# Kernel optimization log

Hardware: AMD Instinct MI355X
Metric: run time of the kernel (lower is better)

The kernel has to match this reference:

```python
import jax, jax.numpy as jnp
import numpy as np
import math

B, S, H = 4, 4096, 64
WINDOW = 2


def setup_inputs() -> dict:
    key = jax.random.key(0)
    ks = jax.random.split(key, 7)
    s = 0.05
    return {
        "feature": jax.random.normal(ks[0], (B, S, H), dtype=jnp.float32),
        "Wq": jax.random.normal(ks[1], (H, H), dtype=jnp.float32) * s,
        "bq": jax.random.normal(ks[2], (H,), dtype=jnp.float32) * s,
        "Wk": jax.random.normal(ks[3], (H, H), dtype=jnp.float32) * s,
        "bk": jax.random.normal(ks[4], (H,), dtype=jnp.float32) * s,
        "Wv": jax.random.normal(ks[5], (H, H), dtype=jnp.float32) * s,
        "bv": jax.random.normal(ks[6], (H,), dtype=jnp.float32) * s,
    }


def reference(feature, Wq, bq, Wk, bk, Wv, bv):
    b, seq, d_k = feature.shape
    # torch nn.Linear: y = x @ W.T + b
    q = feature @ Wq.T + bq  # [B,S,H]
    k = feature @ Wk.T + bk
    v = feature @ Wv.T + bv

    # banded 0/1 mask, |i-j| <= window, then softmax over the FULL row
    # (faithful to the original: zeros outside the band also get exp(0)=1 weight)
    idx = jnp.arange(seq)
    band = (jnp.abs(idx[:, None] - idx[None, :]) <= WINDOW).astype(jnp.float32)  # [S,S]
    weights = jax.nn.softmax(band, axis=-1)  # [S,S]

    # locally-averaged K: weights @ k, shared across batch
    mixed_k = jnp.einsum('st,bth->bsh', weights, k)  # [B,S,H]
    scores = jnp.einsum('bsh,bth->bst', q, mixed_k) / math.sqrt(d_k)  # [B,S,S]
    attn = jax.nn.softmax(scores, axis=-1)
    out = jnp.einsum('bst,bth->bsh', attn, v)  # [B,S,H]
    return out
```

## Files before the change

### kernel.cpp

```cpp
#include <hip/hip_runtime.h>
#include <hip/hip_bf16.h>
#include <math.h>

#define SEQ 4096
#define HD  64
#define NBATCH 4

#define EM1   1.71828182845904523536f
#define INVD5 (1.0f/(4096.f + 5.f*EM1))
#define INVD4 (1.0f/(4096.f + 4.f*EM1))
#define INVD3 (1.0f/(4096.f + 3.f*EM1))

typedef __attribute__((ext_vector_type(8))) short short8;
typedef __attribute__((ext_vector_type(4))) short short4v;
typedef __attribute__((ext_vector_type(4))) float f32x4;

__device__ __forceinline__ f32x4 mfma16(short8 a, short8 b, f32x4 c) {
    return __builtin_amdgcn_mfma_f32_16x16x32_bf16(a, b, c, 0, 0, 0);
}

__device__ __forceinline__ short bfs(float x) {
    __hip_bfloat16 h = __float2bfloat16(x);
    return *(short*)&h;
}

__device__ __forceinline__ float sf(short s) {
    __hip_bfloat16 h;
    *(short*)&h = s;
    return __bfloat162float(h);
}

__device__ __forceinline__ short8 pack8(float4 a, float4 b) {
    short8 r;
    r[0] = bfs(a.x); r[1] = bfs(a.y); r[2] = bfs(a.z); r[3] = bfs(a.w);
    r[4] = bfs(b.x); r[5] = bfs(b.y); r[6] = bfs(b.z); r[7] = bfs(b.w);
    return r;
}

__device__ __forceinline__ float b2f(__hip_bfloat16 h) { return __bfloat162float(h); }

#define WSTR 72

__global__ __launch_bounds__(512, 4) void projm_kernel(
    const float* __restrict__ feat,
    const float* __restrict__ Wq, const float* __restrict__ Wk,
    const float* __restrict__ Wv,
    const float* __restrict__ bq, const float* __restrict__ bk,
    const float* __restrict__ bv,
    __hip_bfloat16* __restrict__ qsb, float* __restrict__ kpart,
    float* __restrict__ vpart, __hip_bfloat16* __restrict__ Mpart,
    float* __restrict__ kedge)
{
    __shared__ __hip_bfloat16 WbL[3 * 64 * WSTR];
    __shared__ __hip_bfloat16 kT[64 * 40];
    __shared__ __hip_bfloat16 vT[64 * 40];
    __shared__ __hip_bfloat16 lvt[64 * 40];
    __shared__ float kred[2][64];
    __shared__ float vred[2][64];

    const int tid  = threadIdx.x;
    const int wv   = tid >> 6, lane = tid & 63;
    const int rh   = wv & 1;
    const int role = wv >> 1;
    const int quad = lane >> 4, ln = lane & 15;
    const int R0 = blockIdx.x * 32;
    const int b  = R0 >> 12;
    const int t0 = R0 & (SEQ - 1);
    const int chunk = blockIdx.x & 127;

    short8 af0, af1;
    const bool hflag = (rh == 0) ? (t0 > 0) : (t0 < SEQ - 32);
    if (role < 3) {
        const float* fp = feat + (size_t)(R0 + rh * 16 + ln) * HD + quad * 8;
        af0 = pack8(*(const float4*)(fp),      *(const float4*)(fp + 4));
        af1 = pack8(*(const float4*)(fp + 32), *(const float4*)(fp + 36));
    } else {
        const int hrow = (rh == 0) ? (t0 - 2 + ln) : (t0 + 32 + ln);
        if (ln < 2 && hflag) {
            const float* fp = feat + ((size_t)(b << 12) + hrow) * HD + quad * 8;
            af0 = pack8(*(const float4*)(fp),      *(const float4*)(fp + 4));
            af1 = pack8(*(const float4*)(fp + 32), *(const float4*)(fp + 36));
        } else {
            #pragma unroll
            for (int j = 0; j < 8; ++j) { af0[j] = 0; af1[j] = 0; }
        }
    }

    {
        const int r = tid >> 3, c = (tid & 7) * 8;
        #pragma unroll
        for (int m = 0; m < 3; ++m) {
            const float* W = (m == 0) ? Wq : (m == 1) ? Wk : Wv;
            const float s = (m == 0) ? 0.125f : 1.f;
            const float* src = W + r * 64 + c;
            float4 a0 = *(const float4*)(src);
            float4 a1 = *(const float4*)(src + 4);
            a0.x*=s; a0.y*=s; a0.z*=s; a0.w*=s;
            a1.x*=s; a1.y*=s; a1.z*=s; a1.w*=s;
            *(short8*)(WbL + m * 64 * WSTR + r * WSTR + c) = pack8(a0, a1);
        }
    }
    __syncthreads();

    if (role == 0) {
        #pragma unroll
        for (int ct = 0; ct < 4; ++ct) {
            const int col = ct * 16 + ln;
            const __hip_bfloat16* wp = WbL + col * WSTR + quad * 8;
            short8 b0 = *(const short8*)(wp);
            short8 b1 = *(const short8*)(wp + 32);
            f32x4 c = {};
            c = mfma16(af0, b0, c);
            c = mfma16(af1, b1, c);
            const float bl = bq[col] * 0.125f;
            #pragma unroll
            for (int rr = 0; rr < 4; ++rr)
                qsb[(size_t)(R0 + rh * 16 + quad * 4 + rr) * HD + col] =
                    __float2bfloat16(c[rr] + bl);
        }
    } else if (role == 1) {
        #pragma unroll
        for (int ct = 0; ct < 4; ++ct) {
            const int col = ct * 16 + ln;
            const __hip_bfloat16* wp = WbL + 64 * WSTR + col * WSTR + quad * 8;
            short8 b0 = *(const short8*)(wp);
            short8 b1 = *(const short8*)(wp + 32);
            f32x4 c = {};
            c = mfma16(af0, b0, c);
            c = mfma16(af1, b1, c);
            float tot = c[0] + c[1] + c[2] + c[3];
            tot += __shfl_xor(tot, 16);
            tot += __shfl_xor(tot, 32);
            if (quad == 0) kred[rh][col] = tot;
            const float bl = bk[col];
            #pragma unroll
            for (int rr = 0; rr < 4; ++rr)
                kT[col * 40 + rh * 16 + quad * 4 + rr] =
                    __float2bfloat16(c[rr] + bl);
        }
    } else if (role == 2) {
        #pragma unroll
        for (int ct = 0; ct < 4; ++ct) {
            const int col = ct * 16 + ln;
            const __hip_bfloat16* wp = WbL + 2 * 64 * WSTR + col * WSTR + quad * 8;
            short8 b0 = *(const short8*)(wp);
            short8 b1 = *(const short8*)(wp + 32);
            f32x4 c = {};
            c = mfma16(af0, b0, c);
            c = mfma16(af1, b1, c);
            float tot = c[0] + c[1] + c[2] + c[3];
            tot += __shfl_xor(tot, 16);
            tot += __shfl_xor(tot, 32);
            if (quad == 0) vred[rh][col] = tot;
            const float bl = bv[col];
            #pragma unroll
            for (int rr = 0; rr < 4; ++rr)
                vT[col * 40 + 2 + rh * 16 + quad * 4 + rr] =
                    __float2bfloat16(c[rr] + bl);
        }
    } else {
        #pragma unroll
        for (int ct = 0; ct < 4; ++ct) {
            const int col = ct * 16 + ln;
            const __hip_bfloat16* wp = WbL + 2 * 64 * WSTR + col * WSTR + quad * 8;
            short8 b0 = *(const short8*)(wp);
            short8 b1 = *(const short8*)(wp + 32);
            f32x4 hc = {};
            hc = mfma16(af0, b0, hc);
            hc = mfma16(af1, b1, hc);
            if (quad == 0) {
                const float bl = bv[col];
                const int base = (rh == 0) ? 0 : 34;
                vT[col * 40 + base]     = __float2bfloat16(hflag ? hc[0] + bl : 0.f);
                vT[col * 40 + base + 1] = __float2bfloat16(hflag ? hc[1] + bl : 0.f);
            }
        }
    }
    __syncthreads();

    if (tid < 64) {
        kpart[(size_t)blockIdx.x * 64 + tid] =
            kred[0][tid] + kred[1][tid] + 32.f * bk[tid];
        vpart[(size_t)blockIdx.x * 64 + tid] =
            vred[0][tid] + vred[1][tid] + 32.f * bv[tid];
    }

    {
        const int h = tid & 63;
        const int tb = (tid >> 6) * 4;
        short4v u0 = *(const short4v*)&vT[h * 40 + tb];
        short4v u1 = *(const short4v*)&vT[h * 40 + tb + 4];
        float w[8];
        #pragma unroll
        for (int j = 0; j < 4; ++j) {
            w[j]     = sf(u0[j]);
            w[j + 4] = sf(u1[j]);
        }
        #pragma unroll
        for (int i = 0; i < 4; ++i)
            lvt[h * 40 + tb + i] =
                __float2bfloat16(w[i] + w[i+1] + w[i+2] + w[i+3] + w[i+4]);
    }

    if (chunk == 0) {
        if (tid < 256) {
            const int t = tid >> 6, h = tid & 63;
            kedge[b * 512 + t * 64 + h] = b2f(kT[h * 40 + t]);
        }
    } else if (chunk == 127) {
        if (tid < 256) {
            const int t = tid >> 6, h = tid & 63;
            kedge[b * 512 + (4 + t) * 64 + h] = b2f(kT[h * 40 + 28 + t]);
        }
    }
    __syncthreads();

    {
        __hip_bfloat16* mp = Mpart + (size_t)(b * 128 + chunk) * 4096;
        const int strip = wv >> 1;
        const int cth   = wv & 1;
        short8 a = *(const short8*)&kT[(strip * 16 + ln) * 40 + quad * 8];
        #pragma unroll
        for (int i = 0; i < 2; ++i) {
            const int ct = cth * 2 + i;
            short8 bb = *(const short8*)&lvt[(ct * 16 + ln) * 40 + quad * 8];
            f32x4 acc = {};
            acc = mfma16(a, bb, acc);
            #pragma unroll
            for (int rr = 0; rr < 4; ++rr)
                mp[(strip * 16 + quad * 4 + rr) * 64 + ct * 16 + ln] =
                    __float2bfloat16(acc[rr]);
        }
    }
}

__global__ __launch_bounds__(256) void redprep_kernel(
    const __hip_bfloat16* __restrict__ Mpart, const float* __restrict__ kpart,
    const float* __restrict__ vpart, const float* __restrict__ kedge,
    __hip_bfloat16* __restrict__ MTm, float* __restrict__ mktotF,
    float* __restrict__ ktotF, float* __restrict__ VDs,
    float* __restrict__ VtotF)
{
    const int b = blockIdx.y, x = blockIdx.x;
    const int tid = threadIdx.x;

    if (x < 32) {
        __shared__ float part[16][132];
        const int gl = tid >> 4;
        const int s  = tid & 15;
        const int e  = x * 128 + gl * 8;
        const __hip_bfloat16* src =
            Mpart + ((size_t)b * 128 + s * 8) * 4096 + e;
        float sum[8] = {0.f,0.f,0.f,0.f,0.f,0.f,0.f,0.f};
        #pragma unroll
        for (int c = 0; c < 8; ++c) {
            short8 v = *(const short8*)(src + (size_t)c * 4096);
            #pragma unroll
            for (int j = 0; j < 8; ++j) sum[j] += sf(v[j]);
        }
        #pragma unroll
        for (int j = 0; j < 8; ++j) part[s][gl * 8 + j] = sum[j];
        __syncthreads();
        if (tid < 128) {
            float t = 0.f;
            #pragma unroll
            for (int ss = 0; ss < 16; ++ss) t += part[ss][tid];
            const int e2 = x * 128 + tid;
            const int h1 = e2 >> 6, h2 = e2 & 63;
            MTm[(size_t)b * 4096 + h2 * 64 + h1] =
                __float2bfloat16((EM1 * INVD5) * t);
        }
        return;
    }

    __shared__ float red[4][64];
    __shared__ float red2[4][64];
    const int g = tid >> 6, h2 = tid & 63;
    {
        float kp = 0.f, vp = 0.f;
        for (int j = 0; j < 32; ++j) {
            kp += kpart[(size_t)(b * 128 + g * 32 + j) * 64 + h2];
            vp += vpart[(size_t)(b * 128 + g * 32 + j) * 64 + h2];
        }
        red[g][h2] = kp;
        red2[g][h2] = vp;
    }
    __syncthreads();
    if (tid < 64) {
        const int hh = tid;
        const float kt = red[0][hh] + red[1][hh] + red[2][hh] + red[3][hh];
        const float vt = red2[0][hh] + red2[1][hh] + red2[2][hh] + red2[3][hh];
        const float e0 = kedge[b * 512 + 0 * 64 + hh];
        const float e1 = kedge[b * 512 + 1 * 64 + hh];
        const float e2 = kedge[b * 512 + 2 * 64 + hh];
        const float e3 = kedge[b * 512 + 3 * 64 + hh];
        const float f0 = kedge[b * 512 + 4 * 64 + hh];
        const float f1 = kedge[b * 512 + 5 * 64 + hh];
        const float f2 = kedge[b * 512 + 6 * 64 + hh];
        const float f3 = kedge[b * 512 + 7 * 64 + hh];
        const float Sint = 5.f*kt - 4.f*e0 - 3.f*e1 - 2.f*e2 - e3
                         - f0 - 2.f*f1 - 3.f*f2 - 4.f*f3;
        const float SlocD = Sint * INVD5
                          + (e0+e1+e2 + f1+f2+f3) * INVD3
                          + (e0+e1+e2+e3 + f0+f1+f2+f3) * INVD4;
        mktotF[b * 64 + hh] = kt * (4092.f*INVD5 + 2.f*INVD4 + 2.f*INVD3) + EM1 * SlocD;
        ktotF[b * 64 + hh]  = kt;
        VDs[b * 64 + hh]    = INVD5 * vt;
        VtotF[b * 64 + hh]  = vt;
    }
}

__global__ __launch_bounds__(128) void out_kernel(
    const __hip_bfloat16* __restrict__ qsb, const __hip_bfloat16* __restrict__ MTm,
    const float* __restrict__ mktotF, const float* __restrict__ ktotF,
    const float* __restrict__ VDs, const float* __restrict__ VtotF,
    float* __restrict__ out)
{
    const int tid = threadIdx.x;
    const int wv = tid >> 6, lane = tid & 63;
    const int quad = lane >> 4, ln = lane & 15;
    const int R0 = blockIdx.x * 16;
    const int b = R0 >> 12;

    short8 qa0, qa1;
    {
        const __hip_bfloat16* qp = qsb + (size_t)(R0 + ln) * HD + quad * 8;
        qa0 = *(const short8*)qp;
        qa1 = *(const short8*)(qp + 32);
    }

    const __hip_bfloat16* mtb = MTm + (size_t)b * 4096;
    f32x4 acc[2];
    #pragma unroll
    for (int i = 0; i < 2; ++i) {
        const int ct = wv * 2 + i;
        short8 b0 = *(const short8*)(mtb + (ct * 16 + ln) * 64 + quad * 8);
        short8 b1 = *(const short8*)(mtb + (ct * 16 + ln) * 64 + 32 + quad * 8);
        f32x4 c = {};
        c = mfma16(qa0, b0, c);
        c = mfma16(qa1, b1, c);
        acc[i] = c;
    }

    short8 mk0, mk1, kt0, kt1;
    #pragma unroll
    for (int j = 0; j < 8; ++j) {
        mk0[j] = bfs(mktotF[b * 64 + quad * 8 + j]);
        mk1[j] = bfs(mktotF[b * 64 + 32 + quad * 8 + j]);
        kt0[j] = bfs(ktotF[b * 64 + quad * 8 + j]);
        kt1[j] = bfs(ktotF[b * 64 + 32 + quad * 8 + j]);
    }
    f32x4 accd = {}, acck = {};
    accd = mfma16(qa0, mk0, accd);
    accd = mfma16(qa1, mk1, accd);
    acck = mfma16(qa0, kt0, acck);
    acck = mfma16(qa1, kt1, acck);

    float vt[2], vd[2];
    #pragma unroll
    for (int i = 0; i < 2; ++i) {
        const int ct = wv * 2 + i;
        vt[i] = VtotF[b * 64 + ct * 16 + ln];
        vd[i] = VDs[b * 64 + ct * 16 + ln];
    }

    float inv[4];
    #pragma unroll
    for (int r = 0; r < 4; ++r) inv[r] = 1.f / (4096.f + accd[r]);

    #pragma unroll
    for (int i = 0; i < 2; ++i)
        #pragma unroll
        for (int r = 0; r < 4; ++r)
            out[(size_t)(R0 + quad * 4 + r) * HD + (wv * 2 + i) * 16 + ln] =
                (vt[i] + acc[i][r] + acck[r] * vd[i]) * inv[r];
}

extern "C" void kernel_launch(void* const* d_in, const int* in_sizes, int n_in,
                              void* d_out, int out_size, void* d_ws, size_t ws_size,
                              hipStream_t stream)
{
    const float* feat = (const float*)d_in[0];
    const float* Wq = (const float*)d_in[1];
    const float* bq = (const float*)d_in[2];
    const float* Wk = (const float*)d_in[3];
    const float* bk = (const float*)d_in[4];
    const float* Wv = (const float*)d_in[5];
    const float* bv = (const float*)d_in[6];
    float* out = (float*)d_out;

    char* ws = (char*)d_ws;
    __hip_bfloat16* qsb    = (__hip_bfloat16*)(ws + 0);
    __hip_bfloat16* Mpart  = (__hip_bfloat16*)(ws + (2u << 20));
    float*          kpart  = (float*)(ws + (6u << 20));
    float*          vpart  = (float*)(ws + (6u << 20) + 131072);
    float*          kedge  = (float*)(ws + (6u << 20) + 262144);
    __hip_bfloat16* MTm    = (__hip_bfloat16*)(ws + (6u << 20) + 270336);
    float*          mktotF = (float*)(ws + (6u << 20) + 303104);
    float*          ktotF  = (float*)(ws + (6u << 20) + 304128);
    float*          VDs    = (float*)(ws + (6u << 20) + 305152);
    float*          VtotF  = (float*)(ws + (6u << 20) + 306176);

    projm_kernel<<<dim3(512), dim3(512), 0, stream>>>(
        feat, Wq, Wk, Wv, bq, bk, bv, qsb, kpart, vpart, Mpart, kedge);
    redprep_kernel<<<dim3(33, NBATCH), dim3(256), 0, stream>>>(
        Mpart, kpart, vpart, kedge, MTm, mktotF, ktotF, VDs, VtotF);
    out_kernel<<<dim3(1024), dim3(128), 0, stream>>>(
        qsb, MTm, mktotF, ktotF, VDs, VtotF, out);
}
```

Before: 79.42 us.

## Fuse reduction kernel into output kernel with per-batch atomic counter barrier

Merges the reduction/prep kernel into the output kernel. The first 65 blocks of each batch reduce Mpart and the k/v partials, then signal a per-batch atomic counter. All blocks spin on that counter before computing outputs. This removes one kernel launch and its gap, but relies on the producer blocks being scheduled while consumers spin. The reduction also becomes less parallel per block, and the counter is reset inside the projection kernel.

```diff
diff --git a/kernel.cpp b/kernel.cpp
--- a/kernel.cpp
+++ b/kernel.cpp
@@ -49,7 +49,7 @@
     const float* __restrict__ bv,
     __hip_bfloat16* __restrict__ qsb, float* __restrict__ kpart,
     float* __restrict__ vpart, __hip_bfloat16* __restrict__ Mpart,
-    float* __restrict__ kedge)
+    float* __restrict__ kedge, unsigned int* __restrict__ doneC)
 {
     __shared__ __hip_bfloat16 WbL[3 * 64 * WSTR];
     __shared__ __hip_bfloat16 kT[64 * 40];
@@ -67,6 +67,8 @@
     const int b  = R0 >> 12;
     const int t0 = R0 & (SEQ - 1);
     const int chunk = blockIdx.x & 127;
+
+    if (blockIdx.x == 0 && tid < 4) doneC[tid] = 0;
 
     short8 af0, af1;
     const bool hflag = (rh == 0) ? (t0 > 0) : (t0 < SEQ - 32);
@@ -234,93 +236,25 @@
     }
 }
 
-__global__ __launch_bounds__(256) void redprep_kernel(
-    const __hip_bfloat16* __restrict__ Mpart, const float* __restrict__ kpart,
-    const float* __restrict__ vpart, const float* __restrict__ kedge,
+__global__ __launch_bounds__(128) void outred_kernel(
+    const __hip_bfloat16* __restrict__ qsb, const __hip_bfloat16* __restrict__ Mpart,
+    const float* __restrict__ kpart, const float* __restrict__ vpart,
+    const float* __restrict__ kedge,
     __hip_bfloat16* __restrict__ MTm, float* __restrict__ mktotF,
     float* __restrict__ ktotF, float* __restrict__ VDs,
-    float* __restrict__ VtotF)
-{
-    const int b = blockIdx.y, x = blockIdx.x;
-    const int tid = threadIdx.x;
-
-    if (x < 32) {
-        __shared__ float part[16][132];
-        const int gl = tid >> 4;
-        const int s  = tid & 15;
-        const int e  = x * 128 + gl * 8;
-        const __hip_bfloat16* src =
-            Mpart + ((size_t)b * 128 + s * 8) * 4096 + e;
-        float sum[8] = {0.f,0.f,0.f,0.f,0.f,0.f,0.f,0.f};
-        #pragma unroll
-        for (int c = 0; c < 8; ++c) {
-            short8 v = *(const short8*)(src + (size_t)c * 4096);
-            #pragma unroll
-            for (int j = 0; j < 8; ++j) sum[j] += sf(v[j]);
-        }
-        #pragma unroll
-        for (int j = 0; j < 8; ++j) part[s][gl * 8 + j] = sum[j];
-        __syncthreads();
-        if (tid < 128) {
-            float t = 0.f;
-            #pragma unroll
-            for (int ss = 0; ss < 16; ++ss) t += part[ss][tid];
-            const int e2 = x * 128 + tid;
-            const int h1 = e2 >> 6, h2 = e2 & 63;
-            MTm[(size_t)b * 4096 + h2 * 64 + h1] =
-                __float2bfloat16((EM1 * INVD5) * t);
-        }
-        return;
-    }
-
-    __shared__ float red[4][64];
-    __shared__ float red2[4][64];
-    const int g = tid >> 6, h2 = tid & 63;
-    {
-        float kp = 0.f, vp = 0.f;
-        for (int j = 0; j < 32; ++j) {
-            kp += kpart[(size_t)(b * 128 + g * 32 + j) * 64 + h2];
-            vp += vpart[(size_t)(b * 128 + g * 32 + j) * 64 + h2];
-        }
-        red[g][h2] = kp;
-        red2[g][h2] = vp;
-    }
-    __syncthreads();
-    if (tid < 64) {
-        const int hh = tid;
-        const float kt = red[0][hh] + red[1][hh] + red[2][hh] + red[3][hh];
-        const float vt = red2[0][hh] + red2[1][hh] + red2[2][hh] + red2[3][hh];
-        const float e0 = kedge[b * 512 + 0 * 64 + hh];
-        const float e1 = kedge[b * 512 + 1 * 64 + hh];
-        const float e2 = kedge[b * 512 + 2 * 64 + hh];
-        const float e3 = kedge[b * 512 + 3 * 64 + hh];
-        const float f0 = kedge[b * 512 + 4 * 64 + hh];
-        const float f1 = kedge[b * 512 + 5 * 64 + hh];
-        const float f2 = kedge[b * 512 + 6 * 64 + hh];
-        const float f3 = kedge[b * 512 + 7 * 64 + hh];
-        const float Sint = 5.f*kt - 4.f*e0 - 3.f*e1 - 2.f*e2 - e3
-                         - f0 - 2.f*f1 - 3.f*f2 - 4.f*f3;
-        const float SlocD = Sint * INVD5
-                          + (e0+e1+e2 + f1+f2+f3) * INVD3
-                          + (e0+e1+e2+e3 + f0+f1+f2+f3) * INVD4;
-        mktotF[b * 64 + hh] = kt * (4092.f*INVD5 + 2.f*INVD4 + 2.f*INVD3) + EM1 * SlocD;
-        ktotF[b * 64 + hh]  = kt;
-        VDs[b * 64 + hh]    = INVD5 * vt;
-        VtotF[b * 64 + hh]  = vt;
-    }
-}
-
-__global__ __launch_bounds__(128) void out_kernel(
-    const __hip_bfloat16* __restrict__ qsb, const __hip_bfloat16* __restrict__ MTm,
-    const float* __restrict__ mktotF, const float* __restrict__ ktotF,
-    const float* __restrict__ VDs, const float* __restrict__ VtotF,
+    float* __restrict__ VtotF, unsigned int* __restrict__ doneC,
     float* __restrict__ out)
 {
+    __shared__ float mred[64];
+    __shared__ float red[2][64];
+    __shared__ float red2[2][64];
+
     const int tid = threadIdx.x;
     const int wv = tid >> 6, lane = tid & 63;
     const int quad = lane >> 4, ln = lane & 15;
     const int R0 = blockIdx.x * 16;
     const int b = R0 >> 12;
+    const int xb = blockIdx.x & 255;
 
     short8 qa0, qa1;
     {
@@ -328,6 +262,72 @@
         qa0 = *(const short8*)qp;
         qa1 = *(const short8*)(qp + 32);
     }
+
+    if (xb < 64) {
+        const int E = xb * 64 + lane;
+        const __hip_bfloat16* src =
+            Mpart + ((size_t)b * 128 + wv * 64) * 4096 + E;
+        float s = 0.f;
+        #pragma unroll
+        for (int c = 0; c < 64; ++c) s += b2f(src[(size_t)c * 4096]);
+        if (wv == 1) mred[lane] = s;
+        __syncthreads();
+        if (wv == 0) {
+            const float t = s + mred[lane];
+            MTm[(size_t)b * 4096 + lane * 64 + xb] =
+                __float2bfloat16((EM1 * INVD5) * t);
+        }
+        if (tid == 0) {
+            __threadfence();
+            __hip_atomic_fetch_add(doneC + b, 1u, __ATOMIC_RELEASE,
+                                   __HIP_MEMORY_SCOPE_AGENT);
+        }
+    } else if (xb == 64) {
+        const int g = wv, hh = lane;
+        float kp = 0.f, vp = 0.f;
+        for (int j = 0; j < 64; ++j) {
+            kp += kpart[(size_t)(b * 128 + g * 64 + j) * 64 + hh];
+            vp += vpart[(size_t)(b * 128 + g * 64 + j) * 64 + hh];
+        }
+        red[g][hh] = kp;
+        red2[g][hh] = vp;
+        __syncthreads();
+        if (tid < 64) {
+            const float kt = red[0][hh] + red[1][hh];
+            const float vt = red2[0][hh] + red2[1][hh];
+            const float e0 = kedge[b * 512 + 0 * 64 + hh];
+            const float e1 = kedge[b * 512 + 1 * 64 + hh];
+            const float e2 = kedge[b * 512 + 2 * 64 + hh];
+            const float e3 = kedge[b * 512 + 3 * 64 + hh];
+            const float f0 = kedge[b * 512 + 4 * 64 + hh];
+            const float f1 = kedge[b * 512 + 5 * 64 + hh];
+            const float f2 = kedge[b * 512 + 6 * 64 + hh];
+            const float f3 = kedge[b * 512 + 7 * 64 + hh];
+            const float Sint = 5.f*kt - 4.f*e0 - 3.f*e1 - 2.f*e2 - e3
+                             - f0 - 2.f*f1 - 3.f*f2 - 4.f*f3;
+            const float SlocD = Sint * INVD5
+                              + (e0+e1+e2 + f1+f2+f3) * INVD3
+                              + (e0+e1+e2+e3 + f0+f1+f2+f3) * INVD4;
+            mktotF[b * 64 + hh] = kt * (4092.f*INVD5 + 2.f*INVD4 + 2.f*INVD3)
+                                + EM1 * SlocD;
+            ktotF[b * 64 + hh]  = kt;
+            VDs[b * 64 + hh]    = INVD5 * vt;
+            VtotF[b * 64 + hh]  = vt;
+        }
+        if (tid == 0) {
+            __threadfence();
+            __hip_atomic_fetch_add(doneC + b, 1u, __ATOMIC_RELEASE,
+                                   __HIP_MEMORY_SCOPE_AGENT);
+        }
+    }
+
+    if (tid == 0) {
+        while (__hip_atomic_load(doneC + b, __ATOMIC_RELAXED,
+                                 __HIP_MEMORY_SCOPE_AGENT) < 65u)
+            __builtin_amdgcn_s_sleep(2);
+    }
+    __syncthreads();
+    __threadfence();
 
     const __hip_bfloat16* mtb = MTm + (size_t)b * 4096;
     f32x4 acc[2];
@@ -400,11 +400,11 @@
     float*          ktotF  = (float*)(ws + (6u << 20) + 304128);
     float*          VDs    = (float*)(ws + (6u << 20) + 305152);
     float*          VtotF  = (float*)(ws + (6u << 20) + 306176);
+    unsigned int*   doneC  = (unsigned int*)(ws + (6u << 20) + 307200);
 
     projm_kernel<<<dim3(512), dim3(512), 0, stream>>>(
-        feat, Wq, Wk, Wv, bq, bk, bv, qsb, kpart, vpart, Mpart, kedge);
-    redprep_kernel<<<dim3(33, NBATCH), dim3(256), 0, stream>>>(
-        Mpart, kpart, vpart, kedge, MTm, mktotF, ktotF, VDs, VtotF);
-    out_kernel<<<dim3(1024), dim3(128), 0, stream>>>(
-        qsb, MTm, mktotF, ktotF, VDs, VtotF, out);
-}
+        feat, Wq, Wk, Wv, bq, bk, bv, qsb, kpart, vpart, Mpart, kedge, doneC);
+    outred_kernel<<<dim3(1024), dim3(128), 0, stream>>>(
+        qsb, Mpart, kpart, vpart, kedge, MTm, mktotF, ktotF, VDs, VtotF,
+        doneC, out);
+}
```

Result: slower. 157.3 us (+98.1%).
